# Kernel optimization log

Hardware: AMD Instinct MI355X
Metric: run time of the kernel (lower is better)

## Reference

```python
import jax, jax.numpy as jnp
import numpy as np
import math

HIDDEN = 384
HEADS = 4
HEAD_DIM = HIDDEN // HEADS
B, T = 8, 2048


def _shift_rel(pos_tensor):
    # pos_tensor: [b, h, t, 2t-1] -> [b, h, t, t] (Transformer-XL shift trick)
    b, h, t, n = pos_tensor.shape
    zero_pad = jnp.zeros((b, h, t, 1), dtype=pos_tensor.dtype)
    padded = jnp.concatenate([zero_pad, pos_tensor], axis=-1)  # [b,h,t,n+1]
    padded = padded.reshape(b, h, n + 1, t)
    shifted = padded[:, :, 1:].reshape(b, h, t, n)
    return shifted[:, :, :, : n // 2 + 1]  # [b,h,t,t]


def setup_inputs() -> dict:
    key = jax.random.key(0)
    ks = jax.random.split(key, 12)
    s = 1.0 / math.sqrt(HIDDEN)
    inp = {
        "hidden_states": jax.random.normal(ks[0], (B, T, HIDDEN), jnp.float32),
        "pos_emb": jax.random.normal(ks[1], (1, 2 * T - 1, HIDDEN), jnp.float32),
        "attention_mask": jnp.ones((B, 1, T), jnp.int32),
        "Wq": jax.random.normal(ks[2], (HIDDEN, HIDDEN), jnp.float32) * s,
        "bq": jnp.zeros((HIDDEN,), jnp.float32),
        "Wk": jax.random.normal(ks[3], (HIDDEN, HIDDEN), jnp.float32) * s,
        "bk": jnp.zeros((HIDDEN,), jnp.float32),
        "Wv": jax.random.normal(ks[4], (HIDDEN, HIDDEN), jnp.float32) * s,
        "bv": jnp.zeros((HIDDEN,), jnp.float32),
        "Wo": jax.random.normal(ks[5], (HIDDEN, HIDDEN), jnp.float32) * s,
        "bo": jnp.zeros((HIDDEN,), jnp.float32),
        "Wpos": jax.random.normal(ks[6], (HIDDEN, HIDDEN), jnp.float32) * s,
        "pos_bias_u": jax.random.normal(ks[7], (HEADS, HEAD_DIM), jnp.float32) * s,
        "pos_bias_v": jax.random.normal(ks[8], (HEADS, HEAD_DIM), jnp.float32) * s,
    }
    return inp


def reference(hidden_states, pos_emb, attention_mask, Wq, bq, Wk, bk, Wv, bv,
              Wo, bo, Wpos, pos_bias_u, pos_bias_v):
    bsz, q_len, _ = hidden_states.shape
    # projections (nn.Linear applies x @ W.T + b; weights here stored as [in, out])
    q = (hidden_states @ Wq + bq).reshape(bsz, q_len, HEADS, HEAD_DIM)
    k = (hidden_states @ Wk + bk).reshape(bsz, q_len, HEADS, HEAD_DIM)
    v = (hidden_states @ Wv + bv).reshape(bsz, q_len, HEADS, HEAD_DIM)
    pos = (pos_emb @ Wpos).reshape(pos_emb.shape[0], -1, HEADS, HEAD_DIM)

    q_u = (q + pos_bias_u).transpose(0, 2, 1, 3)  # [b,h,t,d]
    q_v = (q + pos_bias_v).transpose(0, 2, 1, 3)

    # content score: [b,h,t,t]
    matrix_ac = jnp.einsum('bhqd,bkhd->bhqk', q_u, k)
    # position score: [b,h,t,2t-1] then shift
    matrix_bd = jnp.einsum('bhqd,pnhd->bhqn', q_v, pos)
    matrix_bd = _shift_rel(matrix_bd)

    scores = (matrix_ac + matrix_bd) / math.sqrt(HEAD_DIM)

    mask = (attention_mask[:, None] == 0)  # [b,1,1,t]
    min_val = jnp.finfo(scores.dtype).min
    scores = jnp.where(mask, min_val, scores)
    attn = jax.nn.softmax(scores, axis=-1)
    attn = jnp.where(mask, 0.0, attn)

    out = jnp.einsum('bhqk,bkhd->bqhd', attn, v).reshape(bsz, q_len, HIDDEN)
    return out @ Wo + bo
```

## Files before the change

kernel.cpp:

```cpp
#include <hip/hip_runtime.h>
#include <hip/hip_bf16.h>

#define TSEQ 2048
#define HID 384
#define NHEAD 4
#define HD 96
#define NBATCH 8

using bf16 = __bf16;
typedef bf16 bf16x8 __attribute__((ext_vector_type(8)));
typedef bf16 bf16x4 __attribute__((ext_vector_type(4)));
typedef float f32x4 __attribute__((ext_vector_type(4)));

static __device__ __forceinline__ f32x4 mfma16(bf16x8 a, bf16x8 b, f32x4 c) {
    return __builtin_amdgcn_mfma_f32_16x16x32_bf16(a, b, c, 0, 0, 0);
}

#define LDS_HANDOFF()                                   \
    __builtin_amdgcn_sched_barrier(0x7F);               \
    asm volatile("s_waitcnt lgkmcnt(0)");               \
    __builtin_amdgcn_sched_barrier(0x7F)

#define GL2LDS(g, l) __builtin_amdgcn_global_load_lds(                        \
    (const __attribute__((address_space(1))) unsigned int*)(const void*)(g),  \
    (__attribute__((address_space(3))) unsigned int*)(void*)(l), 16, 0, 0)

__global__ void k_conv8(const float* __restrict__ src, bf16* __restrict__ dst, int n8) {
    int t = blockIdx.x * 256 + threadIdx.x;
    if (t >= n8) return;
    const float4* s4 = reinterpret_cast<const float4*>(src);
    float4 a = s4[2 * t], b = s4[2 * t + 1];
    bf16x8 o;
    o[0] = (bf16)a.x; o[1] = (bf16)a.y; o[2] = (bf16)a.z; o[3] = (bf16)a.w;
    o[4] = (bf16)b.x; o[5] = (bf16)b.y; o[6] = (bf16)b.z; o[7] = (bf16)b.w;
    *reinterpret_cast<bf16x8*>(dst + 8 * t) = o;
}

__global__ void k_convT(const float* __restrict__ W, bf16* __restrict__ WT) {
    int t = blockIdx.x * 256 + threadIdx.x;
    int n = t / HID, k = t % HID;
    WT[t] = (bf16)W[(size_t)k * HID + n];
}

__launch_bounds__(256, 2)
__global__ void k_proj(const bf16* __restrict__ X, const bf16* __restrict__ P,
                       const bf16* __restrict__ wqT, const bf16* __restrict__ wkT,
                       const bf16* __restrict__ wvT, const bf16* __restrict__ wpT,
                       const float* __restrict__ bq, const float* __restrict__ bk,
                       const float* __restrict__ bv,
                       const float* __restrict__ pbu, const float* __restrict__ pbv,
                       bf16* __restrict__ qu, bf16* __restrict__ qv,
                       bf16* __restrict__ kws, bf16* __restrict__ vt,
                       bf16* __restrict__ pp) {
    __shared__ bf16 wt_lds[96][392];
    const float SC = 0.10206207262f;
    int mat = blockIdx.z;
    int m0 = blockIdx.x * 64;
    if (mat == 3 && m0 >= 4095) return;
    int n0 = blockIdx.y * 96;
    const bf16* A  = (mat == 3) ? P : X;
    const bf16* WT = (mat == 0) ? wqT : (mat == 1) ? wkT : (mat == 2) ? wvT : wpT;
    int tid = threadIdx.x;
    #pragma unroll
    for (int s = 0; s < 18; ++s) {
        int cc = tid + 256 * s;
        int r = cc / 48, ch = cc % 48;
        *reinterpret_cast<int4*>(&wt_lds[r][ch * 8]) =
            *reinterpret_cast<const int4*>(WT + (size_t)(n0 + r) * HID + ch * 8);
    }
    __syncthreads();
    int lane = tid & 63, w = tid >> 6;
    int c = lane & 15, g = lane >> 4;
    int arow = m0 + 16 * w + c;
    if (mat == 3 && arow > 4095) arow = 4095;
    const bf16* Abase = A + (size_t)arow * HID + 8 * g;
    f32x4 acc[6] = {};
    for (int ks = 0; ks < 12; ++ks) {
        bf16x8 a = *reinterpret_cast<const bf16x8*>(Abase + 32 * ks);
        #pragma unroll
        for (int jt = 0; jt < 6; ++jt) {
            bf16x8 b = *reinterpret_cast<const bf16x8*>(&wt_lds[16 * jt + c][32 * ks + 8 * g]);
            acc[jt] = mfma16(a, b, acc[jt]);
        }
    }
    int h = blockIdx.y;
    int rbase = m0 + 16 * w + 4 * g;
    if (mat == 0) {
        #pragma unroll
        for (int jt = 0; jt < 6; ++jt) {
            int n = n0 + 16 * jt + c;
            int d = 16 * jt + c;
            float bb = bq[n], bu = pbu[n], bvv = pbv[n];
            #pragma unroll
            for (int j = 0; j < 4; ++j) {
                int m = rbase + j;
                int b_ = m >> 11, t = m & 2047;
                size_t o = (((size_t)(b_ * NHEAD + h)) * TSEQ + t) * HD + d;
                float q = acc[jt][j] + bb;
                qu[o] = (bf16)((q + bu) * SC);
                qv[o] = (bf16)((q + bvv) * SC);
            }
        }
    } else if (mat == 1) {
        #pragma unroll
        for (int jt = 0; jt < 6; ++jt) {
            int n = n0 + 16 * jt + c;
            int d = 16 * jt + c;
            float bb = bk[n];
            #pragma unroll
            for (int j = 0; j < 4; ++j) {
                int m = rbase + j;
                int b_ = m >> 11, t = m & 2047;
                size_t o = (((size_t)(b_ * NHEAD + h)) * TSEQ + t) * HD + d;
                kws[o] = (bf16)(acc[jt][j] + bb);
            }
        }
    } else if (mat == 2) {
        #pragma unroll
        for (int jt = 0; jt < 6; ++jt) {
            int d = 16 * jt + c;
            float bb = bv[n0 + 16 * jt + c];
            int m = rbase;
            int b_ = m >> 11, t0 = m & 2047;
            size_t o = (((size_t)(b_ * NHEAD + h)) * HD + d) * TSEQ + t0;
            bf16x4 pk;
            #pragma unroll
            for (int j = 0; j < 4; ++j) pk[j] = (bf16)(acc[jt][j] + bb);
            *reinterpret_cast<bf16x4*>(vt + o) = pk;
        }
    } else {
        #pragma unroll
        for (int jt = 0; jt < 6; ++jt) {
            int d = 16 * jt + c;
            #pragma unroll
            for (int j = 0; j < 4; ++j) {
                int m = rbase + j;
                if (m < 4095) {
                    size_t o = ((size_t)h * 4096 + m) * HD + d;
                    pp[o] = (bf16)acc[jt][j];
                }
            }
        }
    }
}

__launch_bounds__(256, 4)
__global__ void k_attn(const bf16* __restrict__ qu, const bf16* __restrict__ qv,
                       const bf16* __restrict__ kws, const bf16* __restrict__ vt,
                       const bf16* __restrict__ pp, const int* __restrict__ mask,
                       bf16* __restrict__ out) {
    __shared__ bf16 k_lds[64][96];
    __shared__ bf16 vt_lds[96][64];
    __shared__ bf16 wp_lds[4][16][104];

    int bid = blockIdx.x;
    int x = bid & 7, j5 = bid >> 3;
    int h = x & 3;
    int b_ = (x >> 2) * 4 + (j5 >> 5);
    int qb = j5 & 31;
    int bh = b_ * NHEAD + h;
    int q0 = qb * 64;

    int tid = threadIdx.x, lane = tid & 63, w = tid >> 6;
    int c = lane & 15, g = lane >> 4;
    const int n_base0 = TSEQ - 1 - 63 - q0;
    const float L2E = 1.44269504089f;
    int sw = 48 - 16 * w;

    int cc0 = tid, cc1 = tid + 256, cc2 = tid + 512;
    int kr0 = cc0 / 12, kc0 = cc0 % 12;
    int kr1 = cc1 / 12, kc1 = cc1 % 12;
    int kr2 = cc2 / 12, kc2 = cc2 % 12;
    int kO0 = kr0 * HD + (kc0 ^ (kr0 & 3)) * 8;
    int kO1 = kr1 * HD + (kc1 ^ (kr1 & 3)) * 8;
    int kO2 = kr2 * HD + (kc2 ^ (kr2 & 3)) * 8;
    bf16* k_flat = &k_lds[0][0];
    bf16* kL0 = k_flat + (size_t)(0 * 256 + 64 * w) * 8;
    bf16* kL1 = k_flat + (size_t)(1 * 256 + 64 * w) * 8;
    bf16* kL2 = k_flat + (size_t)(2 * 256 + 64 * w) * 8;
    int vr0 = cc0 >> 3, vc0 = cc0 & 7;
    int vr1 = cc1 >> 3, vc1 = cc1 & 7;
    int vr2 = cc2 >> 3, vc2 = cc2 & 7;
    int vO0 = vr0 * TSEQ + (vc0 ^ (vr0 & 7)) * 8;
    int vO1 = vr1 * TSEQ + (vc1 ^ (vr1 & 7)) * 8;
    int vO2 = vr2 * TSEQ + (vc2 ^ (vr2 & 7)) * 8;
    bf16* vt_flat = &vt_lds[0][0];
    bf16* vL0 = vt_flat + (size_t)(0 * 256 + 64 * w) * 8;
    bf16* vL1 = vt_flat + (size_t)(1 * 256 + 64 * w) * 8;
    bf16* vL2 = vt_flat + (size_t)(2 * 256 + 64 * w) * 8;

    const bf16* kbP = kws + (size_t)bh * TSEQ * HD;
    const bf16* vbP = vt + (size_t)bh * HD * TSEQ;
    const bf16* pbP = pp + (size_t)h * 4096 * HD;
    const int*  mbP = mask + b_ * TSEQ;

    bf16x8 qu_f[3], qv_f[3];
    {
        size_t rowbase = ((size_t)bh * TSEQ + q0 + 16 * w + c) * HD + 8 * g;
        #pragma unroll
        for (int ds = 0; ds < 3; ++ds) {
            qu_f[ds] = *reinterpret_cast<const bf16x8*>(qu + rowbase + 32 * ds);
            qv_f[ds] = *reinterpret_cast<const bf16x8*>(qv + rowbase + 32 * ds);
        }
    }

    f32x4 acc_o[6] = {};
    float mrow = -3.0e38f, lrow = 0.f;
    f32x4 wc;
    int   mkreg;

    {
        GL2LDS(vbP + vO0, vL0);
        GL2LDS(vbP + vO1, vL1);
        GL2LDS(vbP + vO2, vL2);
        GL2LDS(kbP + kO0, kL0);
        GL2LDS(kbP + kO1, kL1);
        GL2LDS(kbP + kO2, kL2);
        mkreg = mbP[lane];

        int wb = n_base0 + sw;
        {
            f32x4 w0 = {};
            const bf16* p0 = pbP + (size_t)(wb + c) * HD + 8 * g;
            #pragma unroll
            for (int ds = 0; ds < 3; ++ds)
                w0 = mfma16(*reinterpret_cast<const bf16x8*>(p0 + 32 * ds), qv_f[ds], w0);
            #pragma unroll
            for (int j = 0; j < 4; ++j)
                wp_lds[w][c][4 * g + j + c + 1] = (bf16)w0[j];
        }
        {
            f32x4 w1 = {}, w2 = {};
            const bf16* p1 = pbP + (size_t)(wb + 16 + c) * HD + 8 * g;
            const bf16* p2 = pbP + (size_t)(wb + 32 + c) * HD + 8 * g;
            #pragma unroll
            for (int ds = 0; ds < 3; ++ds) {
                w1 = mfma16(*reinterpret_cast<const bf16x8*>(p1 + 32 * ds), qv_f[ds], w1);
                w2 = mfma16(*reinterpret_cast<const bf16x8*>(p2 + 32 * ds), qv_f[ds], w2);
            }
            #pragma unroll
            for (int j = 0; j < 4; ++j) {
                wp_lds[w][c][16 + 4 * g + j + c + 1] = (bf16)w1[j];
                wp_lds[w][c][32 + 4 * g + j + c + 1] = (bf16)w2[j];
            }
        }
        {
            f32x4 w3 = {}, w4 = {};
            const bf16* p3 = pbP + (size_t)(wb + 48 + c) * HD + 8 * g;
            const bf16* p4 = pbP + (size_t)(wb + 64 + c) * HD + 8 * g;
            #pragma unroll
            for (int ds = 0; ds < 3; ++ds) {
                w3 = mfma16(*reinterpret_cast<const bf16x8*>(p3 + 32 * ds), qv_f[ds], w3);
                w4 = mfma16(*reinterpret_cast<const bf16x8*>(p4 + 32 * ds), qv_f[ds], w4);
            }
            #pragma unroll
            for (int j = 0; j < 4; ++j) {
                wp_lds[w][c][48 + 4 * g + j + c + 1] = (bf16)w3[j];
                wp_lds[w][c][64 + 4 * g + j + c + 1] = (bf16)w4[j];
            }
            wc = w4;
        }
    }
    __syncthreads();

    for (int kt = 0; kt < 32; ++kt) {
        unsigned long long bm = __ballot(mkreg != 0);

        bf16x4 wv0 = *reinterpret_cast<const bf16x4*>(&wp_lds[w][c][4 * g + 16]);
        bf16x4 wv1 = *reinterpret_cast<const bf16x4*>(&wp_lds[w][c][16 + 4 * g + 16]);
        bf16x4 wv2 = *reinterpret_cast<const bf16x4*>(&wp_lds[w][c][32 + 4 * g + 16]);
        bf16x4 wv3 = *reinterpret_cast<const bf16x4*>(&wp_lds[w][c][48 + 4 * g + 16]);

        __builtin_amdgcn_s_setprio(1);
        f32x4 acc_s[4] = {};
        #pragma unroll
        for (int ds = 0; ds < 3; ++ds) {
            #pragma unroll
            for (int t = 0; t < 4; ++t) {
                bf16x8 a = *reinterpret_cast<const bf16x8*>(
                    &k_lds[16 * t + c][(((4 * ds + g) ^ (c & 3)) * 8)]);
                acc_s[t] = mfma16(a, qu_f[ds], acc_s[t]);
            }
        }
        __builtin_amdgcn_s_setprio(0);

        acc_s[0][0] += (float)wv0[0]; acc_s[0][1] += (float)wv0[1];
        acc_s[0][2] += (float)wv0[2]; acc_s[0][3] += (float)wv0[3];
        acc_s[1][0] += (float)wv1[0]; acc_s[1][1] += (float)wv1[1];
        acc_s[1][2] += (float)wv1[2]; acc_s[1][3] += (float)wv1[3];
        acc_s[2][0] += (float)wv2[0]; acc_s[2][1] += (float)wv2[1];
        acc_s[2][2] += (float)wv2[2]; acc_s[2][3] += (float)wv2[3];
        acc_s[3][0] += (float)wv3[0]; acc_s[3][1] += (float)wv3[1];
        acc_s[3][2] += (float)wv3[2]; acc_s[3][3] += (float)wv3[3];
        if (bm != ~0ull) {
            #pragma unroll
            for (int t = 0; t < 4; ++t)
                #pragma unroll
                for (int j = 0; j < 4; ++j)
                    if (!((bm >> (16 * t + 4 * g + j)) & 1)) acc_s[t][j] = -3.0e38f;
        }
        float pm = acc_s[0][0];
        #pragma unroll
        for (int t = 0; t < 4; ++t)
            #pragma unroll
            for (int j = 0; j < 4; ++j) pm = fmaxf(pm, acc_s[t][j]);
        pm = fmaxf(pm, __shfl_xor(pm, 16));
        pm = fmaxf(pm, __shfl_xor(pm, 32));
        if (!__all(pm <= mrow + 8.0f)) {
            float mnew = fmaxf(mrow, pm);
            float alpha = exp2f((mrow - mnew) * L2E);
            mrow = mnew; lrow *= alpha;
            #pragma unroll
            for (int ot = 0; ot < 6; ++ot) acc_o[ot] *= alpha;
        }
        float rs = 0.f;
        #pragma unroll
        for (int t = 0; t < 4; ++t)
            #pragma unroll
            for (int j = 0; j < 4; ++j) {
                float p = exp2f((acc_s[t][j] - mrow) * L2E);
                acc_s[t][j] = p; rs += p;
            }
        rs += __shfl_xor(rs, 16);
        rs += __shfl_xor(rs, 32);
        lrow += rs;

        #pragma unroll
        for (int t = 0; t < 4; ++t) {
            bf16x4 pk;
            #pragma unroll
            for (int j = 0; j < 4; ++j) pk[j] = (bf16)acc_s[t][j];
            *reinterpret_cast<bf16x4*>(&wp_lds[w][c][16 * t + 4 * g]) = pk;
        }
        LDS_HANDOFF();

        __builtin_amdgcn_s_setprio(1);
        #pragma unroll
        for (int ds = 0; ds < 2; ++ds) {
            bf16x8 pb_ = *reinterpret_cast<const bf16x8*>(&wp_lds[w][c][32 * ds + 8 * g]);
            #pragma unroll
            for (int ot = 0; ot < 6; ++ot) {
                int rr = 16 * ot + c;
                bf16x8 a = *reinterpret_cast<const bf16x8*>(
                    &vt_lds[rr][((4 * ds + g) ^ (rr & 7)) * 8]);
                acc_o[ot] = mfma16(a, pb_, acc_o[ot]);
            }
        }
        __builtin_amdgcn_s_setprio(0);

        if (kt < 31) {
            __syncthreads();

            int k0n = (kt + 1) * 64;
            const bf16* kb = kbP + (size_t)k0n * HD;
            const bf16* vb = vbP + k0n;
            GL2LDS(vb + vO0, vL0);
            GL2LDS(vb + vO1, vL1);
            GL2LDS(vb + vO2, vL2);
            GL2LDS(kb + kO0, kL0);
            GL2LDS(kb + kO1, kL1);
            GL2LDS(kb + kO2, kL2);
            mkreg = mbP[k0n + lane];

            int wb = n_base0 + 64 * (kt + 1) + sw;
            #pragma unroll
            for (int j = 0; j < 4; ++j)
                wp_lds[w][c][4 * g + j + c + 1] = (bf16)wc[j];
            {
                f32x4 w1 = {}, w2 = {};
                const bf16* p1 = pbP + (size_t)(wb + 16 + c) * HD + 8 * g;
                const bf16* p2 = pbP + (size_t)(wb + 32 + c) * HD + 8 * g;
                __builtin_amdgcn_s_setprio(1);
                #pragma unroll
                for (int ds = 0; ds < 3; ++ds) {
                    w1 = mfma16(*reinterpret_cast<const bf16x8*>(p1 + 32 * ds), qv_f[ds], w1);
                    w2 = mfma16(*reinterpret_cast<const bf16x8*>(p2 + 32 * ds), qv_f[ds], w2);
                }
                __builtin_amdgcn_s_setprio(0);
                #pragma unroll
                for (int j = 0; j < 4; ++j) {
                    wp_lds[w][c][16 + 4 * g + j + c + 1] = (bf16)w1[j];
                    wp_lds[w][c][32 + 4 * g + j + c + 1] = (bf16)w2[j];
                }
            }
            {
                f32x4 w3 = {}, w4 = {};
                const bf16* p3 = pbP + (size_t)(wb + 48 + c) * HD + 8 * g;
                const bf16* p4 = pbP + (size_t)(wb + 64 + c) * HD + 8 * g;
                __builtin_amdgcn_s_setprio(1);
                #pragma unroll
                for (int ds = 0; ds < 3; ++ds) {
                    w3 = mfma16(*reinterpret_cast<const bf16x8*>(p3 + 32 * ds), qv_f[ds], w3);
                    w4 = mfma16(*reinterpret_cast<const bf16x8*>(p4 + 32 * ds), qv_f[ds], w4);
                }
                __builtin_amdgcn_s_setprio(0);
                #pragma unroll
                for (int j = 0; j < 4; ++j) {
                    wp_lds[w][c][48 + 4 * g + j + c + 1] = (bf16)w3[j];
                    wp_lds[w][c][64 + 4 * g + j + c + 1] = (bf16)w4[j];
                }
                wc = w4;
            }

            __syncthreads();
        }
    }

    float inv = 1.0f / lrow;
    size_t m = (size_t)b_ * TSEQ + q0 + 16 * w + c;
    bf16* ob = out + m * HID + h * HD + 4 * g;
    #pragma unroll
    for (int ot = 0; ot < 6; ++ot) {
        bf16x4 pk;
        #pragma unroll
        for (int j = 0; j < 4; ++j) pk[j] = (bf16)(acc_o[ot][j] * inv);
        *reinterpret_cast<bf16x4*>(&ob[16 * ot]) = pk;
    }
}

__launch_bounds__(256, 2)
__global__ void k_oproj(const bf16* __restrict__ A, const bf16* __restrict__ WT,
                        const float* __restrict__ bias, float* __restrict__ out) {
    __shared__ bf16 wt_lds[96][392];
    int m0 = blockIdx.x * 64, n0 = blockIdx.y * 96;
    int tid = threadIdx.x;
    #pragma unroll
    for (int s = 0; s < 18; ++s) {
        int cc = tid + 256 * s;
        int r = cc / 48, ch = cc % 48;
        *reinterpret_cast<int4*>(&wt_lds[r][ch * 8]) =
            *reinterpret_cast<const int4*>(WT + (size_t)(n0 + r) * HID + ch * 8);
    }
    __syncthreads();
    int lane = tid & 63, w = tid >> 6;
    int c = lane & 15, g = lane >> 4;
    const bf16* Abase = A + (size_t)(m0 + 16 * w + c) * HID + 8 * g;
    f32x4 acc[6] = {};
    for (int ks = 0; ks < 12; ++ks) {
        bf16x8 a = *reinterpret_cast<const bf16x8*>(Abase + 32 * ks);
        #pragma unroll
        for (int jt = 0; jt < 6; ++jt) {
            bf16x8 b = *reinterpret_cast<const bf16x8*>(&wt_lds[16 * jt + c][32 * ks + 8 * g]);
            acc[jt] = mfma16(a, b, acc[jt]);
        }
    }
    int rbase = m0 + 16 * w + 4 * g;
    #pragma unroll
    for (int jt = 0; jt < 6; ++jt) {
        int n = n0 + 16 * jt + c;
        float bb = bias[n];
        #pragma unroll
        for (int j = 0; j < 4; ++j)
            out[(size_t)(rbase + j) * HID + n] = acc[jt][j] + bb;
    }
}

extern "C" void kernel_launch(void* const* d_in, const int* in_sizes, int n_in,
                              void* d_out, int out_size, void* d_ws, size_t ws_size,
                              hipStream_t stream) {
    const float* hs  = (const float*)d_in[0];
    const float* pe  = (const float*)d_in[1];
    const int*   msk = (const int*)d_in[2];
    const float* Wq  = (const float*)d_in[3];
    const float* bq  = (const float*)d_in[4];
    const float* Wk  = (const float*)d_in[5];
    const float* bk  = (const float*)d_in[6];
    const float* Wv  = (const float*)d_in[7];
    const float* bv  = (const float*)d_in[8];
    const float* Wo  = (const float*)d_in[9];
    const float* bo  = (const float*)d_in[10];
    const float* Wp  = (const float*)d_in[11];
    const float* pbu = (const float*)d_in[12];
    const float* pbv = (const float*)d_in[13];

    char* ws = (char*)d_ws;
    size_t off = 0;
    auto alloc = [&](size_t b) { char* p = ws + off; off += (b + 255) & ~(size_t)255; return p; };
    bf16* Xb  = (bf16*)alloc((size_t)16384 * HID * 2);
    bf16* Pb  = (bf16*)alloc((size_t)4096 * HID * 2);
    bf16* wqT = (bf16*)alloc((size_t)HID * HID * 2);
    bf16* wkT = (bf16*)alloc((size_t)HID * HID * 2);
    bf16* wvT = (bf16*)alloc((size_t)HID * HID * 2);
    bf16* woT = (bf16*)alloc((size_t)HID * HID * 2);
    bf16* wpT = (bf16*)alloc((size_t)HID * HID * 2);
    bf16* qu  = (bf16*)alloc((size_t)NBATCH * NHEAD * TSEQ * HD * 2);
    bf16* qv  = (bf16*)alloc((size_t)NBATCH * NHEAD * TSEQ * HD * 2);
    bf16* kws = (bf16*)alloc((size_t)NBATCH * NHEAD * TSEQ * HD * 2);
    bf16* vt  = (bf16*)alloc((size_t)NBATCH * NHEAD * TSEQ * HD * 2);
    bf16* pp  = (bf16*)alloc((size_t)NHEAD * 4096 * HD * 2 + 65536);
    bf16* ao  = (bf16*)alloc((size_t)16384 * HID * 2);

    k_conv8<<<3072, 256, 0, stream>>>(hs, Xb, 786432);
    k_conv8<<<768, 256, 0, stream>>>(pe, Pb, 196560);
    k_convT<<<576, 256, 0, stream>>>(Wq, wqT);
    k_convT<<<576, 256, 0, stream>>>(Wk, wkT);
    k_convT<<<576, 256, 0, stream>>>(Wv, wvT);
    k_convT<<<576, 256, 0, stream>>>(Wo, woT);
    k_convT<<<576, 256, 0, stream>>>(Wp, wpT);
    k_proj<<<dim3(256, 4, 4), 256, 0, stream>>>(Xb, Pb, wqT, wkT, wvT, wpT,
                                                bq, bk, bv, pbu, pbv,
                                                qu, qv, kws, vt, pp);
    k_attn<<<1024, 256, 0, stream>>>(qu, qv, kws, vt, pp, msk, ao);
    k_oproj<<<dim3(256, 4), 256, 0, stream>>>(ao, woT, bo, (float*)d_out);
}
```

Baseline: 298.6 us.

## Double attention query tile to 128 rows with 8 waves sharing K/V tiles

The attention kernel now uses 512-thread blocks with 8 waves covering 128 query rows instead of 4 waves covering 64, and launches half as many blocks. Each loaded K and V^T tile in LDS is reused by twice as many query rows, and the cooperative global-to-LDS loads are redistributed so each wave issues three loads instead of six. This cuts global/L2 traffic for K and V, but halves the grid to 512 blocks, which may lower load balance and occupancy on a 256-CU device, and raises LDS use per block for the enlarged positional scratch buffer.

```diff
diff --git a/kernel.cpp b/kernel.cpp
--- a/kernel.cpp
+++ b/kernel.cpp
@@ -144,50 +144,46 @@
     }
 }
 
-__launch_bounds__(256, 4)
+__launch_bounds__(512, 4)
 __global__ void k_attn(const bf16* __restrict__ qu, const bf16* __restrict__ qv,
                        const bf16* __restrict__ kws, const bf16* __restrict__ vt,
                        const bf16* __restrict__ pp, const int* __restrict__ mask,
                        bf16* __restrict__ out) {
     __shared__ bf16 k_lds[64][96];
     __shared__ bf16 vt_lds[96][64];
-    __shared__ bf16 wp_lds[4][16][104];
+    __shared__ bf16 wp_lds[8][16][104];
 
     int bid = blockIdx.x;
-    int x = bid & 7, j5 = bid >> 3;
+    int x = bid & 7, j6 = bid >> 3;
     int h = x & 3;
-    int b_ = (x >> 2) * 4 + (j5 >> 5);
-    int qb = j5 & 31;
+    int b_ = (x >> 2) * 4 + (j6 >> 4);
+    int qb = j6 & 15;
     int bh = b_ * NHEAD + h;
-    int q0 = qb * 64;
+    int q0 = qb * 128;
 
     int tid = threadIdx.x, lane = tid & 63, w = tid >> 6;
     int c = lane & 15, g = lane >> 4;
-    const int n_base0 = TSEQ - 1 - 63 - q0;
+    const int n_base0 = TSEQ - 1 - 127 - q0;
     const float L2E = 1.44269504089f;
-    int sw = 48 - 16 * w;
-
-    int cc0 = tid, cc1 = tid + 256, cc2 = tid + 512;
-    int kr0 = cc0 / 12, kc0 = cc0 % 12;
-    int kr1 = cc1 / 12, kc1 = cc1 % 12;
-    int kr2 = cc2 / 12, kc2 = cc2 % 12;
+    int sw = 112 - 16 * w;
+
+    bf16* k_flat = &k_lds[0][0];
+    bf16* vt_flat = &vt_lds[0][0];
+    int ch0 = 64 * w + lane;
+    int kr0 = ch0 / 12, kc0 = ch0 % 12;
     int kO0 = kr0 * HD + (kc0 ^ (kr0 & 3)) * 8;
-    int kO1 = kr1 * HD + (kc1 ^ (kr1 & 3)) * 8;
-    int kO2 = kr2 * HD + (kc2 ^ (kr2 & 3)) * 8;
-    bf16* k_flat = &k_lds[0][0];
-    bf16* kL0 = k_flat + (size_t)(0 * 256 + 64 * w) * 8;
-    bf16* kL1 = k_flat + (size_t)(1 * 256 + 64 * w) * 8;
-    bf16* kL2 = k_flat + (size_t)(2 * 256 + 64 * w) * 8;
-    int vr0 = cc0 >> 3, vc0 = cc0 & 7;
-    int vr1 = cc1 >> 3, vc1 = cc1 & 7;
-    int vr2 = cc2 >> 3, vc2 = cc2 & 7;
-    int vO0 = vr0 * TSEQ + (vc0 ^ (vr0 & 7)) * 8;
-    int vO1 = vr1 * TSEQ + (vc1 ^ (vr1 & 7)) * 8;
+    bf16* L0 = k_flat + w * 512;
+    bool s1K = (w < 4);
+    int reg1 = s1K ? (8 + w) : (w - 4);
+    int ch1 = 64 * reg1 + lane;
+    int o1;
+    if (s1K) { int r = ch1 / 12, cch = ch1 % 12; o1 = r * HD + (cch ^ (r & 3)) * 8; }
+    else     { int r = ch1 >> 3, cch = ch1 & 7;  o1 = r * TSEQ + (cch ^ (r & 7)) * 8; }
+    bf16* L1 = s1K ? (k_flat + (8 + w) * 512) : (vt_flat + (w - 4) * 512);
+    int ch2 = 64 * (w + 4) + lane;
+    int vr2 = ch2 >> 3, vc2 = ch2 & 7;
     int vO2 = vr2 * TSEQ + (vc2 ^ (vr2 & 7)) * 8;
-    bf16* vt_flat = &vt_lds[0][0];
-    bf16* vL0 = vt_flat + (size_t)(0 * 256 + 64 * w) * 8;
-    bf16* vL1 = vt_flat + (size_t)(1 * 256 + 64 * w) * 8;
-    bf16* vL2 = vt_flat + (size_t)(2 * 256 + 64 * w) * 8;
+    bf16* L2 = vt_flat + (w + 4) * 512;
 
     const bf16* kbP = kws + (size_t)bh * TSEQ * HD;
     const bf16* vbP = vt + (size_t)bh * HD * TSEQ;
@@ -210,12 +206,9 @@
     int   mkreg;
 
     {
-        GL2LDS(vbP + vO0, vL0);
-        GL2LDS(vbP + vO1, vL1);
-        GL2LDS(vbP + vO2, vL2);
-        GL2LDS(kbP + kO0, kL0);
-        GL2LDS(kbP + kO1, kL1);
-        GL2LDS(kbP + kO2, kL2);
+        GL2LDS(kbP + kO0, L0);
+        GL2LDS((s1K ? kbP : vbP) + o1, L1);
+        GL2LDS(vbP + vO2, L2);
         mkreg = mbP[lane];
 
         int wb = n_base0 + sw;
@@ -354,12 +347,9 @@
             int k0n = (kt + 1) * 64;
             const bf16* kb = kbP + (size_t)k0n * HD;
             const bf16* vb = vbP + k0n;
-            GL2LDS(vb + vO0, vL0);
-            GL2LDS(vb + vO1, vL1);
-            GL2LDS(vb + vO2, vL2);
-            GL2LDS(kb + kO0, kL0);
-            GL2LDS(kb + kO1, kL1);
-            GL2LDS(kb + kO2, kL2);
+            GL2LDS(kb + kO0, L0);
+            GL2LDS((s1K ? kb : vb) + o1, L1);
+            GL2LDS(vb + vO2, L2);
             mkreg = mbP[k0n + lane];
 
             int wb = n_base0 + 64 * (kt + 1) + sw;
@@ -500,6 +490,6 @@
     k_proj<<<dim3(256, 4, 4), 256, 0, stream>>>(Xb, Pb, wqT, wkT, wvT, wpT,
                                                 bq, bk, bv, pbu, pbv,
                                                 qu, qv, kws, vt, pp);
-    k_attn<<<1024, 256, 0, stream>>>(qu, qv, kws, vt, pp, msk, ao);
+    k_attn<<<512, 512, 0, stream>>>(qu, qv, kws, vt, pp, msk, ao);
     k_oproj<<<dim3(256, 4), 256, 0, stream>>>(ao, woT, bo, (float*)d_out);
 }
```

New measurement: 302.1 us. Within noise of the previous version (+1.2%).
